# Kernel tuning notes

Hardware: AMD Instinct MI355X
Metric: run time of the kernel (lower is better)

## Reference

```python
import jax, jax.numpy as jnp
import numpy as np

DIM = 1024
SCALE = DIM ** (-0.5)
TEMPERATURE = 1.0


def setup_inputs() -> dict:
    key = jax.random.key(0)
    ks = jax.random.split(key, 7)
    B, N, D = 8, 4096, DIM
    s = 1.0 / np.sqrt(D)
    return {
        "x": jax.random.normal(ks[0], (B, N, D), dtype=jnp.float32),
        "Wq": jax.random.normal(ks[1], (D, D), dtype=jnp.float32) * s,
        "bq": jax.random.normal(ks[2], (D,), dtype=jnp.float32) * 0.01,
        "Wk": jax.random.normal(ks[3], (D, D), dtype=jnp.float32) * s,
        "bk": jax.random.normal(ks[4], (D,), dtype=jnp.float32) * 0.01,
        "Wv": jax.random.normal(ks[5], (D, D), dtype=jnp.float32) * s,
        "bv": jax.random.normal(ks[6], (D,), dtype=jnp.float32) * 0.01,
    }


def reference(x, Wq, bq, Wk, bk, Wv, bv):
    B, N, D = x.shape
    # adaptive_avg_pool1d from N -> N//2 with N even == mean over adjacent pairs
    q_input = x.reshape(B, N // 2, 2, D).mean(axis=2)  # [B, N/2, D]
    # torch Linear: y = x @ W.T + b
    q = jnp.einsum("bmd,ed->bme", q_input, Wq) + bq      # [B, N/2, D]
    k = jnp.einsum("bnd,ed->bne", x, Wk) + bk            # [B, N, D]
    v = jnp.einsum("bnd,ed->bne", x, Wv) + bv            # [B, N, D]
    attn = jnp.einsum("bmd,bnd->bmn", q, k) * SCALE      # [B, N/2, N]
    attn = jax.nn.softmax(attn * TEMPERATURE, axis=-1)
    k_out = jnp.einsum("bmn,bnd->bmd", attn, v)          # [B, N/2, D]
    return (q, k_out, k_out)
```

## Files before the change

kernel.cpp:

```cpp
#include <hip/hip_runtime.h>
#include <hip/hip_bf16.h>
#include <cstddef>

typedef __attribute__((ext_vector_type(8))) short s16x8;
typedef __attribute__((ext_vector_type(4))) short s16x4;
typedef __attribute__((ext_vector_type(4))) float f32x4;

#define MFMA_BF16(a, b, c) __builtin_amdgcn_mfma_f32_16x16x32_bf16((a), (b), (c), 0, 0, 0)

__device__ __forceinline__ short f2bf(float f) {
    union { float f; unsigned u; } cv; cv.f = f;
    unsigned u = cv.u;
    unsigned r = (u + 0x7FFFu + ((u >> 16) & 1u)) >> 16;
    return (short)r;
}
__device__ __forceinline__ float bf2f(unsigned short u) {
    union { unsigned u; float f; } cv; cv.u = ((unsigned)u) << 16; return cv.f;
}

__device__ __forceinline__ void gl16(const void* g, void* l) {
    __builtin_amdgcn_global_load_lds(
        (const __attribute__((address_space(1))) void*)g,
        (__attribute__((address_space(3))) void*)l, 16, 0, 0);
}

template <int MODE>
__global__ __launch_bounds__(256, 2) void gemm_bf(
    const void* __restrict__ Ap, const short* __restrict__ Bp,
    const float* __restrict__ bias, const float* __restrict__ lvec,
    void* __restrict__ Cp, void* __restrict__ Cp2)
{
    constexpr int NT  = (MODE == 4) ? 64 : 16;
    constexpr int LDA = (MODE == 4) ? 4096 : 1024;
    constexpr int LDB = (MODE == 4) ? 4096 : 1024;

    __shared__ short As[128 * 64];
    __shared__ short Bs[128 * 64];
    const int tid = threadIdx.x;

    int bx, by, z;
    if constexpr (MODE == 1 || MODE == 3 || MODE == 4 || MODE == 5) {
        const int n = blockIdx.x;
        constexpr int NBY = (MODE == 1) ? 8 : 16;
        z = n & 7; const int m = n >> 3; by = m % NBY; bx = m / NBY;
    } else { bx = blockIdx.x; by = blockIdx.y; z = blockIdx.z; }

    const int w = tid >> 6, l = tid & 63, l15 = l & 15, lhi = l >> 4;
    const int wy = w >> 1, wx = w & 1;
    const int X = (l15 & 7) << 3;
    const int lr8 = l >> 3, cb = l & 7, scb = cb ^ lr8;

    size_t arow0 = (size_t)by * 128, brow0 = (size_t)bx * 128;
    if constexpr (MODE == 3 || MODE == 4 || MODE == 5) arow0 += (size_t)z * 2048;
    if constexpr (MODE == 1 || MODE == 3 || MODE == 5) brow0 += (size_t)z * 4096;
    if constexpr (MODE == 4) brow0 += (size_t)z * 1024;

    const short* Ab = (const short*)Ap;
    const float* Af = (const float*)Ap;

    const short* gA = Ab + (arow0 + w * 32 + lr8) * (size_t)LDA + scb * 8;
    const short* gB = Bp + (brow0 + w * 32 + lr8) * (size_t)LDB + scb * 8;

    f32x4 acc[4][4];
    #pragma unroll
    for (int m = 0; m < 4; ++m)
        #pragma unroll
        for (int n = 0; n < 4; ++n) acc[m][n] = (f32x4){0.f, 0.f, 0.f, 0.f};

    const int r0b = tid >> 3, cb8 = (tid & 7) * 8;
    const int r0f = tid >> 4, kcs = tid & 15;

    for (int kt = 0; kt < NT; ++kt) {
        #pragma unroll
        for (int i = 0; i < 4; ++i)
            gl16(gB + (size_t)(i * 8) * LDB + kt * 64, &Bs[(w * 32 + i * 8) * 64]);
        if constexpr (MODE == 2) {
            #pragma unroll
            for (int p = 0; p < 4; ++p) {
                const int r = r0b + p * 32;
                const size_t g = (arow0 + r) * 2048 + kt * 64 + cb8;
                s16x8 u0 = *(const s16x8*)(Ab + g);
                s16x8 u1 = *(const s16x8*)(Ab + g + 1024);
                s16x8 o;
                #pragma unroll
                for (int j = 0; j < 8; ++j)
                    o[j] = f2bf(0.5f * (bf2f((unsigned short)u0[j]) + bf2f((unsigned short)u1[j])));
                *(s16x8*)&As[r * 64 + (cb8 ^ ((r & 7) * 8))] = o;
            }
        } else if constexpr (MODE == 3) {
            const int k0 = kt * 64 + kcs * 4;
            #pragma unroll
            for (int p = 0; p < 8; ++p) {
                const int r = r0f + p * 16;
                float4 u = *(const float4*)(Af + (arow0 + r) * 1024 + k0);
                s16x4 sa = { f2bf(u.x * 0.03125f), f2bf(u.y * 0.03125f),
                             f2bf(u.z * 0.03125f), f2bf(u.w * 0.03125f) };
                *(s16x4*)&As[r * 64 + ((kcs * 4) ^ ((r & 7) * 8))] = sa;
            }
        } else {
            #pragma unroll
            for (int i = 0; i < 4; ++i)
                gl16(gA + (size_t)(i * 8) * LDA + kt * 64, &As[(w * 32 + i * 8) * 64]);
        }
        __syncthreads();
        #pragma unroll
        for (int kk = 0; kk < 2; ++kk) {
            const int e = (kk * 32 + lhi * 8) ^ X;
            s16x8 af[4], bfr[4];
            #pragma unroll
            for (int m = 0; m < 4; ++m)
                af[m] = *(const s16x8*)&As[(wy * 64 + m * 16 + l15) * 64 + e];
            #pragma unroll
            for (int n = 0; n < 4; ++n)
                bfr[n] = *(const s16x8*)&Bs[(wx * 64 + n * 16 + l15) * 64 + e];
            #pragma unroll
            for (int m = 0; m < 4; ++m)
                #pragma unroll
                for (int n = 0; n < 4; ++n)
                    acc[m][n] = MFMA_BF16(af[m], bfr[n], acc[m][n]);
        }
        __syncthreads();
    }

    #pragma unroll
    for (int m = 0; m < 4; ++m) {
        #pragma unroll
        for (int j = 0; j < 4; ++j) {
            const int rl = wy * 64 + m * 16 + lhi * 4 + j;
            const int grow = by * 128 + rl;
            float radd = 0.f, rmul = 1.f;
            if constexpr (MODE == 1) radd = bias[grow];
            if constexpr (MODE == 4) rmul = 1.0f / lvec[(size_t)z * 2048 + grow];
            #pragma unroll
            for (int n = 0; n < 4; ++n) {
                const int cl = wx * 64 + n * 16 + l15;
                const int gcol = bx * 128 + cl;
                float v = acc[m][n][j];
                if constexpr (MODE == 0) {
                    ((short*)Cp)[(size_t)grow * 1024 + gcol] = f2bf(v + bias[gcol]);
                } else if constexpr (MODE == 1) {
                    ((short*)Cp)[(size_t)z * 4194304 + (size_t)grow * 4096 + gcol] = f2bf(v + radd);
                } else if constexpr (MODE == 2) {
                    const float qv = v + bias[gcol];
                    ((float*)Cp)[(size_t)grow * 1024 + gcol] = qv;
                    if (Cp2 != nullptr)
                        ((short*)Cp2)[(size_t)grow * 1024 + gcol] = f2bf(qv * 0.03125f);
                } else if constexpr (MODE == 3 || MODE == 5) {
                    ((short*)Cp)[(size_t)z * 8388608 + (size_t)grow * 4096 + gcol] = f2bf(v);
                } else {
                    const size_t o = ((size_t)z * 2048 + grow) * 1024 + gcol;
                    const float ov = v * rmul;
                    ((float*)Cp)[o] = ov;
                    ((float*)Cp2)[o] = ov;
                }
            }
        }
    }
}

template <int MODE>
__global__ __launch_bounds__(256, 2) void gemm_f32(
    const float* __restrict__ Ap, const float* __restrict__ Bp,
    const float* __restrict__ bias, void* __restrict__ Cp, void* __restrict__ Cp2)
{
    constexpr int LDA = (MODE == 2) ? 2048 : 1024;
    __shared__ short As[128 * 64];
    __shared__ short Bs[128 * 64];
    const int tid = threadIdx.x;
    const int bx = blockIdx.x, by = blockIdx.y, z = blockIdx.z;
    const int w = tid >> 6, l = tid & 63, l15 = l & 15, lhi = l >> 4;
    const int wy = w >> 1, wx = w & 1;
    const int X = (l15 & 7) << 3;

    size_t arow0 = (size_t)by * 128, brow0 = (size_t)bx * 128;
    if constexpr (MODE == 1) brow0 += (size_t)z * 4096;

    f32x4 acc[4][4];
    #pragma unroll
    for (int m = 0; m < 4; ++m)
        #pragma unroll
        for (int n = 0; n < 4; ++n) acc[m][n] = (f32x4){0.f, 0.f, 0.f, 0.f};

    const int r0f = tid >> 4, kcs = tid & 15;
    float4 ra[8], ra2[8], rb[8];

    auto load_tile = [&](int kt) {
        const int k0 = kt * 64 + kcs * 4;
        #pragma unroll
        for (int p = 0; p < 8; ++p) {
            const int r = r0f + p * 16;
            if constexpr (MODE == 2) {
                const float* s0 = Ap + (arow0 + r) * (size_t)LDA + k0;
                ra[p] = *(const float4*)s0;
                ra2[p] = *(const float4*)(s0 + 1024);
            } else {
                ra[p] = *(const float4*)(Ap + (arow0 + r) * (size_t)LDA + k0);
            }
            rb[p] = *(const float4*)(Bp + (brow0 + r) * (size_t)1024 + k0);
        }
    };

    load_tile(0);
    for (int kt = 0; kt < 16; ++kt) {
        #pragma unroll
        for (int p = 0; p < 8; ++p) {
            const int r = r0f + p * 16;
            const int e = (kcs * 4) ^ ((r & 7) << 3);
            float ax, ay, az, aw;
            if constexpr (MODE == 2) {
                ax = 0.5f * (ra[p].x + ra2[p].x); ay = 0.5f * (ra[p].y + ra2[p].y);
                az = 0.5f * (ra[p].z + ra2[p].z); aw = 0.5f * (ra[p].w + ra2[p].w);
            } else {
                ax = ra[p].x; ay = ra[p].y; az = ra[p].z; aw = ra[p].w;
            }
            s16x4 sa = { f2bf(ax), f2bf(ay), f2bf(az), f2bf(aw) };
            *(s16x4*)&As[r * 64 + e] = sa;
            s16x4 sb = { f2bf(rb[p].x), f2bf(rb[p].y), f2bf(rb[p].z), f2bf(rb[p].w) };
            *(s16x4*)&Bs[r * 64 + e] = sb;
        }
        if (kt + 1 < 16) load_tile(kt + 1);
        __syncthreads();
        #pragma unroll
        for (int kk = 0; kk < 2; ++kk) {
            const int e = (kk * 32 + lhi * 8) ^ X;
            s16x8 af[4], bfr[4];
            #pragma unroll
            for (int m = 0; m < 4; ++m)
                af[m] = *(const s16x8*)&As[(wy * 64 + m * 16 + l15) * 64 + e];
            #pragma unroll
            for (int n = 0; n < 4; ++n)
                bfr[n] = *(const s16x8*)&Bs[(wx * 64 + n * 16 + l15) * 64 + e];
            #pragma unroll
            for (int m = 0; m < 4; ++m)
                #pragma unroll
                for (int n = 0; n < 4; ++n)
                    acc[m][n] = MFMA_BF16(af[m], bfr[n], acc[m][n]);
        }
        __syncthreads();
    }

    #pragma unroll
    for (int m = 0; m < 4; ++m) {
        #pragma unroll
        for (int j = 0; j < 4; ++j) {
            const int rl = wy * 64 + m * 16 + lhi * 4 + j;
            const int grow = by * 128 + rl;
            const float radd = (MODE == 1) ? bias[grow] : 0.f;
            #pragma unroll
            for (int n = 0; n < 4; ++n) {
                const int cl = wx * 64 + n * 16 + l15;
                const int gcol = bx * 128 + cl;
                float v = acc[m][n][j];
                if constexpr (MODE == 0) {
                    ((short*)Cp)[(size_t)grow * 1024 + gcol] = f2bf(v + bias[gcol]);
                } else if constexpr (MODE == 1) {
                    ((short*)Cp)[(size_t)z * 4194304 + (size_t)grow * 4096 + gcol] = f2bf(v + radd);
                } else {
                    const float q = v + bias[gcol];
                    ((float*)Cp)[(size_t)grow * 1024 + gcol] = q;
                    ((short*)Cp2)[(size_t)grow * 1024 + gcol] = f2bf(q * 0.03125f);
                }
            }
        }
    }
}

__global__ __launch_bounds__(256, 4) void convert_x(const float* __restrict__ x,
                                                    short* __restrict__ xb)
{
    const size_t i0 = ((size_t)blockIdx.x * 256 + threadIdx.x) * 8;
    float4 a = *(const float4*)(x + i0), b = *(const float4*)(x + i0 + 4);
    s16x8 o = { f2bf(a.x), f2bf(a.y), f2bf(a.z), f2bf(a.w),
                f2bf(b.x), f2bf(b.y), f2bf(b.z), f2bf(b.w) };
    *(s16x8*)(xb + i0) = o;
}

__global__ __launch_bounds__(256, 4) void convert_w(
    const float* __restrict__ Wq, const float* __restrict__ Wk,
    const float* __restrict__ Wv, short* __restrict__ Wb)
{
    const int gid = blockIdx.x * 256 + threadIdx.x;
    const int seg = gid >> 17;
    const size_t off = (size_t)(gid & 131071) * 8;
    const float* s = (seg == 0) ? Wq : ((seg == 1) ? Wk : Wv);
    float4 a = *(const float4*)(s + off), b = *(const float4*)(s + off + 4);
    s16x8 o = { f2bf(a.x), f2bf(a.y), f2bf(a.z), f2bf(a.w),
                f2bf(b.x), f2bf(b.y), f2bf(b.z), f2bf(b.w) };
    *(s16x8*)(Wb + (size_t)seg * 1048576 + off) = o;
}

__global__ __launch_bounds__(256, 4) void softmax_rows(
    const unsigned short* __restrict__ Sin, unsigned short* __restrict__ Pout,
    float* __restrict__ lvec)
{
    const int w = threadIdx.x >> 6, l = threadIdx.x & 63;
    const int row = blockIdx.x * 4 + w;
    const unsigned short* rp = Sin + (size_t)row * 4096;
    unsigned short* wp = Pout + (size_t)row * 4096;

    s16x8 v[8];
    #pragma unroll
    for (int c = 0; c < 8; ++c)
        v[c] = *(const s16x8*)(rp + (c * 64 + l) * 8);

    float mx = -1e30f;
    #pragma unroll
    for (int c = 0; c < 8; ++c)
        #pragma unroll
        for (int j = 0; j < 8; ++j)
            mx = fmaxf(mx, bf2f((unsigned short)v[c][j]));
    #pragma unroll
    for (int d = 1; d < 64; d <<= 1) mx = fmaxf(mx, __shfl_xor(mx, d));

    float sum = 0.f;
    #pragma unroll
    for (int c = 0; c < 8; ++c) {
        #pragma unroll
        for (int j = 0; j < 8; ++j) {
            const float p = __expf(bf2f((unsigned short)v[c][j]) - mx);
            sum += p;
            v[c][j] = f2bf(p);
        }
    }
    #pragma unroll
    for (int d = 1; d < 64; d <<= 1) sum += __shfl_xor(sum, d);

    #pragma unroll
    for (int c = 0; c < 8; ++c)
        *(s16x8*)(wp + (c * 64 + l) * 8) = v[c];
    if (l == 0) lvec[row] = sum;
}

__global__ __launch_bounds__(256, 4) void dup_out(
    const float4* __restrict__ O, float4* __restrict__ o1, float4* __restrict__ o2)
{
    const size_t i0 = (size_t)blockIdx.x * 256 + threadIdx.x;
    #pragma unroll
    for (int p = 0; p < 4; ++p) {
        const size_t i = i0 + (size_t)p * 1048576;
        const float4 t = O[i];
        o1[i] = t;
        o2[i] = t;
    }
}

extern "C" void kernel_launch(void* const* d_in, const int* in_sizes, int n_in,
                              void* d_out, int out_size, void* d_ws, size_t ws_size,
                              hipStream_t stream) {
    const float* x  = (const float*)d_in[0];
    const float* Wq = (const float*)d_in[1];
    const float* bq = (const float*)d_in[2];
    const float* Wk = (const float*)d_in[3];
    const float* bk = (const float*)d_in[4];
    const float* Wv = (const float*)d_in[5];
    const float* bv = (const float*)d_in[6];

    float* out   = (float*)d_out;
    float* q_out = out;
    float* out1  = out + (size_t)16777216;
    float* out2  = out + (size_t)33554432;
    short* Smat  = (short*)out1;

    const unsigned long long NEED_A2 = 241434624ULL;
    const unsigned long long NEED_A1 = 207683584ULL;

    if ((unsigned long long)ws_size >= NEED_A2) {
        short* xb  = (short*)d_ws;
        short* Wb  = xb + (size_t)33554432;
        short* kws = Wb + (size_t)3145728;
        short* vT  = kws + (size_t)33554432;
        short* qs  = vT + (size_t)33554432;
        float* lws = (float*)(qs + (size_t)16777216);
        unsigned short* Pws = (unsigned short*)d_ws;

        convert_x<<<dim3(16384, 1, 1), 256, 0, stream>>>(x, xb);
        convert_w<<<dim3(1536, 1, 1), 256, 0, stream>>>(Wq, Wk, Wv, Wb);
        gemm_bf<0><<<dim3(8, 256, 1), 256, 0, stream>>>(xb, Wb + 1048576, bk, nullptr, (void*)kws, nullptr);
        gemm_bf<1><<<dim3(2048, 1, 1), 256, 0, stream>>>(Wb + 2097152, xb, bv, nullptr, (void*)vT, nullptr);
        gemm_bf<2><<<dim3(8, 128, 1), 256, 0, stream>>>(xb, Wb, bq, nullptr, (void*)q_out, (void*)qs);
        gemm_bf<5><<<dim3(4096, 1, 1), 256, 0, stream>>>(qs, kws, nullptr, nullptr, (void*)Smat, nullptr);
        softmax_rows<<<dim3(4096, 1, 1), 256, 0, stream>>>((const unsigned short*)Smat, Pws, lws);
        gemm_bf<4><<<dim3(1024, 1, 1), 256, 0, stream>>>(Pws, vT, nullptr, lws, (void*)out1, (void*)out2);
    } else if ((unsigned long long)ws_size >= NEED_A1) {
        short* xb  = (short*)d_ws;
        short* Wb  = xb + (size_t)33554432;
        short* kws = Wb + (size_t)3145728;
        short* vT  = kws + (size_t)33554432;
        float* lws = (float*)((char*)d_ws + 207618048ULL);
        unsigned short* Pws = (unsigned short*)d_ws;

        convert_x<<<dim3(16384, 1, 1), 256, 0, stream>>>(x, xb);
        convert_w<<<dim3(1536, 1, 1), 256, 0, stream>>>(Wq, Wk, Wv, Wb);
        gemm_bf<0><<<dim3(8, 256, 1), 256, 0, stream>>>(xb, Wb + 1048576, bk, nullptr, (void*)kws, nullptr);
        gemm_bf<1><<<dim3(2048, 1, 1), 256, 0, stream>>>(Wb + 2097152, xb, bv, nullptr, (void*)vT, nullptr);
        gemm_bf<2><<<dim3(8, 128, 1), 256, 0, stream>>>(xb, Wb, bq, nullptr, (void*)q_out, nullptr);
        gemm_bf<3><<<dim3(4096, 1, 1), 256, 0, stream>>>(q_out, kws, nullptr, nullptr, (void*)Smat, nullptr);
        softmax_rows<<<dim3(4096, 1, 1), 256, 0, stream>>>((const unsigned short*)Smat, Pws, lws);
        gemm_bf<4><<<dim3(1024, 1, 1), 256, 0, stream>>>(Pws, vT, nullptr, lws, (void*)out1, (void*)out2);
    } else {
        short* kws = (short*)d_ws;
        short* vT  = kws + (size_t)33554432;
        short* qs  = vT + (size_t)33554432;
        float* lws = (float*)((char*)d_ws + 167772160ULL);
        float* Ows = (float*)d_ws;

        gemm_f32<0><<<dim3(8, 256, 1), 256, 0, stream>>>(x, Wk, bk, (void*)kws, nullptr);
        gemm_f32<1><<<dim3(32, 8, 8), 256, 0, stream>>>(Wv, x, bv, (void*)vT, nullptr);
        gemm_f32<2><<<dim3(8, 128, 1), 256, 0, stream>>>(x, Wq, bq, (void*)q_out, (void*)qs);
        gemm_bf<5><<<dim3(4096, 1, 1), 256, 0, stream>>>(qs, kws, nullptr, nullptr, (void*)Smat, nullptr);
        softmax_rows<<<dim3(4096, 1, 1), 256, 0, stream>>>((const unsigned short*)Smat, (unsigned short*)Smat, lws);
        gemm_bf<4><<<dim3(1024, 1, 1), 256, 0, stream>>>(Smat, vT, nullptr, lws, (void*)Ows, (void*)Ows);
        dup_out<<<dim3(4096, 1, 1), 256, 0, stream>>>((const float4*)Ows, (float4*)out1, (float4*)out2);
    }
}
```

Baseline: 652.8 us.

## Add 256x256-tile double-buffered bf16 GEMM for attention score and PV products

Introduces a 512-thread GEMM kernel with 256x256 output tiles, a double-buffered LDS staging pipeline fed by direct global-to-LDS loads, and XOR-swizzled LDS addressing. It replaces the 128-tile kernels for the Q·K^T score product and the normalized P·V output product on the large-workspace path. The larger tiles raise operand reuse per loaded byte and cut global traffic. In exchange the kernel uses about 128KB of LDS and many accumulator registers, which limits occupancy. The P·V grid is only 256 blocks, so load balance across CUs may suffer.

```diff
diff --git a/kernel.cpp b/kernel.cpp
--- a/kernel.cpp
+++ b/kernel.cpp
@@ -22,6 +22,123 @@
     __builtin_amdgcn_global_load_lds(
         (const __attribute__((address_space(1))) void*)g,
         (__attribute__((address_space(3))) void*)l, 16, 0, 0);
+}
+
+template <int MODE>
+__global__ __launch_bounds__(512, 2) void gemm256(
+    const short* __restrict__ Ap, const short* __restrict__ Bp,
+    const float* __restrict__ lvec, void* __restrict__ Cp, void* __restrict__ Cp2)
+{
+    constexpr int NT  = (MODE == 1) ? 64 : 16;
+    constexpr int LDA = (MODE == 1) ? 4096 : 1024;
+    constexpr int LDB = (MODE == 1) ? 4096 : 1024;
+    constexpr int NBX = (MODE == 1) ? 4 : 16;
+
+    __shared__ short As[2][256 * 64];
+    __shared__ short Bs[2][256 * 64];
+
+    const int tid = threadIdx.x;
+    const int n = blockIdx.x;
+    const int z = n & 7;
+    const int m_ = n >> 3;
+    const int by = m_ & 7, bx = m_ >> 3;
+    (void)NBX;
+
+    const int w = tid >> 6, l = tid & 63;
+    const int l15 = l & 15, lhi = l >> 4;
+    const int wr = w >> 2, wc = w & 3;
+    const int X = (l15 & 7) << 3;
+    const int lr8 = l >> 3, cb = l & 7, scb = cb ^ lr8;
+
+    const size_t arow0 = (size_t)z * 2048 + (size_t)by * 256;
+    const size_t brow0 = (size_t)((MODE == 1) ? z * 1024 : z * 4096) + (size_t)bx * 256;
+
+    const short* gA = Ap + (arow0 + w * 8 + lr8) * (size_t)LDA + scb * 8;
+    const short* gB = Bp + (brow0 + w * 8 + lr8) * (size_t)LDB + scb * 8;
+
+    f32x4 acc[8][4];
+    #pragma unroll
+    for (int mm = 0; mm < 8; ++mm)
+        #pragma unroll
+        for (int nn = 0; nn < 4; ++nn) acc[mm][nn] = (f32x4){0.f, 0.f, 0.f, 0.f};
+
+    auto STAGE = [&](int c, int t) {
+        const size_t ko = (size_t)t * 64;
+        #pragma unroll
+        for (int i = 0; i < 4; ++i)
+            gl16(gA + (size_t)(i * 64) * LDA + ko, &As[c][(i * 64 + w * 8) * 64]);
+        #pragma unroll
+        for (int i = 0; i < 4; ++i)
+            gl16(gB + (size_t)(i * 64) * LDB + ko, &Bs[c][(i * 64 + w * 8) * 64]);
+    };
+
+    auto COMPUTE = [&](int c) {
+        #pragma unroll
+        for (int kk = 0; kk < 2; ++kk) {
+            const int e = (kk * 32 + lhi * 8) ^ X;
+            s16x8 af[8], bfr[4];
+            #pragma unroll
+            for (int mm = 0; mm < 8; ++mm)
+                af[mm] = *(const s16x8*)&As[c][(wr * 128 + mm * 16 + l15) * 64 + e];
+            #pragma unroll
+            for (int nn = 0; nn < 4; ++nn)
+                bfr[nn] = *(const s16x8*)&Bs[c][(wc * 64 + nn * 16 + l15) * 64 + e];
+            #pragma unroll
+            for (int mm = 0; mm < 8; ++mm)
+                #pragma unroll
+                for (int nn = 0; nn < 4; ++nn)
+                    acc[mm][nn] = MFMA_BF16(af[mm], bfr[nn], acc[mm][nn]);
+        }
+    };
+
+    STAGE(0, 0);
+    STAGE(1, 1);
+    asm volatile("s_waitcnt vmcnt(8)" ::: "memory");
+    __builtin_amdgcn_s_barrier();
+    asm volatile("" ::: "memory");
+
+    for (int t = 0; t < NT - 2; ++t) {
+        const int c = t & 1;
+        COMPUTE(c);
+        asm volatile("s_waitcnt lgkmcnt(0)" ::: "memory");
+        __builtin_amdgcn_s_barrier();
+        asm volatile("" ::: "memory");
+        __builtin_amdgcn_sched_barrier(0);
+        STAGE(c, t + 2);
+        asm volatile("s_waitcnt vmcnt(8)" ::: "memory");
+        __builtin_amdgcn_s_barrier();
+        asm volatile("" ::: "memory");
+    }
+    COMPUTE((NT - 2) & 1);
+    asm volatile("s_waitcnt vmcnt(0)" ::: "memory");
+    __builtin_amdgcn_s_barrier();
+    asm volatile("" ::: "memory");
+    COMPUTE((NT - 1) & 1);
+
+    #pragma unroll
+    for (int mm = 0; mm < 8; ++mm) {
+        #pragma unroll
+        for (int j = 0; j < 4; ++j) {
+            const int gr = by * 256 + wr * 128 + mm * 16 + lhi * 4 + j;
+            if constexpr (MODE == 0) {
+                #pragma unroll
+                for (int nn = 0; nn < 4; ++nn) {
+                    const int gc = bx * 256 + wc * 64 + nn * 16 + l15;
+                    ((short*)Cp)[(size_t)z * 8388608 + (size_t)gr * 4096 + gc] = f2bf(acc[mm][nn][j]);
+                }
+            } else {
+                const float rmul = 1.0f / lvec[(size_t)z * 2048 + gr];
+                #pragma unroll
+                for (int nn = 0; nn < 4; ++nn) {
+                    const int gc = bx * 256 + wc * 64 + nn * 16 + l15;
+                    const size_t o = ((size_t)z * 2048 + gr) * 1024 + gc;
+                    const float ov = acc[mm][nn][j] * rmul;
+                    ((float*)Cp)[o] = ov;
+                    ((float*)Cp2)[o] = ov;
+                }
+            }
+        }
+    }
 }
 
 template <int MODE>
@@ -378,9 +495,9 @@
         gemm_bf<0><<<dim3(8, 256, 1), 256, 0, stream>>>(xb, Wb + 1048576, bk, nullptr, (void*)kws, nullptr);
         gemm_bf<1><<<dim3(2048, 1, 1), 256, 0, stream>>>(Wb + 2097152, xb, bv, nullptr, (void*)vT, nullptr);
         gemm_bf<2><<<dim3(8, 128, 1), 256, 0, stream>>>(xb, Wb, bq, nullptr, (void*)q_out, (void*)qs);
-        gemm_bf<5><<<dim3(4096, 1, 1), 256, 0, stream>>>(qs, kws, nullptr, nullptr, (void*)Smat, nullptr);
+        gemm256<0><<<dim3(1024, 1, 1), 512, 0, stream>>>(qs, kws, nullptr, (void*)Smat, nullptr);
         softmax_rows<<<dim3(4096, 1, 1), 256, 0, stream>>>((const unsigned short*)Smat, Pws, lws);
-        gemm_bf<4><<<dim3(1024, 1, 1), 256, 0, stream>>>(Pws, vT, nullptr, lws, (void*)out1, (void*)out2);
+        gemm256<1><<<dim3(256, 1, 1), 512, 0, stream>>>((const short*)Pws, vT, lws, (void*)out1, (void*)out2);
     } else if ((unsigned long long)ws_size >= NEED_A1) {
         short* xb  = (short*)d_ws;
         short* Wb  = xb + (size_t)33554432;
```

Result: slower. 674.9 us (+3.4%).

## Add double-buffered LDS GEMM kernel and use it for K, V, S, PV GEMMs

Applied to the files above, without the earlier changes.

Introduces gemm_db, a variant of the bf16 MFMA GEMM that keeps two LDS buffers for A and B tiles. It issues async global-to-LDS loads for the next K tile before computing the current one, with one barrier per iteration. The goal is to overlap memory latency with MFMA work. The cost is double the LDS (64 KB per block), which may limit occupancy to two blocks per CU or fewer. The Q projection GEMM keeps the old kernel.

```diff
diff --git a/kernel.cpp b/kernel.cpp
--- a/kernel.cpp
+++ b/kernel.cpp
@@ -22,6 +22,114 @@
     __builtin_amdgcn_global_load_lds(
         (const __attribute__((address_space(1))) void*)g,
         (__attribute__((address_space(3))) void*)l, 16, 0, 0);
+}
+
+template <int MODE>
+__global__ __launch_bounds__(256, 2) void gemm_db(
+    const short* __restrict__ Ap, const short* __restrict__ Bp,
+    const float* __restrict__ bias, const float* __restrict__ lvec,
+    void* __restrict__ Cp, void* __restrict__ Cp2)
+{
+    constexpr int NT  = (MODE == 4) ? 64 : 16;
+    constexpr int LDA = (MODE == 4) ? 4096 : 1024;
+    constexpr int LDB = (MODE == 4) ? 4096 : 1024;
+
+    __shared__ short As[2][128 * 64];
+    __shared__ short Bs[2][128 * 64];
+
+    const int tid = threadIdx.x;
+    int bx, by, z;
+    if constexpr (MODE == 1 || MODE == 4 || MODE == 5) {
+        const int n = blockIdx.x;
+        constexpr int NBY = (MODE == 1) ? 8 : 16;
+        z = n & 7; const int m = n >> 3; by = m % NBY; bx = m / NBY;
+    } else { bx = blockIdx.x; by = blockIdx.y; z = 0; }
+
+    const int w = tid >> 6, l = tid & 63, l15 = l & 15, lhi = l >> 4;
+    const int wy = w >> 1, wx = w & 1;
+    const int X = (l15 & 7) << 3;
+    const int lr8 = l >> 3, cb = l & 7, scb = cb ^ lr8;
+
+    size_t arow0 = (size_t)by * 128, brow0 = (size_t)bx * 128;
+    if constexpr (MODE == 4 || MODE == 5) arow0 += (size_t)z * 2048;
+    if constexpr (MODE == 1 || MODE == 5) brow0 += (size_t)z * 4096;
+    if constexpr (MODE == 4) brow0 += (size_t)z * 1024;
+
+    const short* gA = Ap + (arow0 + w * 32 + lr8) * (size_t)LDA + scb * 8;
+    const short* gB = Bp + (brow0 + w * 32 + lr8) * (size_t)LDB + scb * 8;
+
+    f32x4 acc[4][4];
+    #pragma unroll
+    for (int m = 0; m < 4; ++m)
+        #pragma unroll
+        for (int n = 0; n < 4; ++n) acc[m][n] = (f32x4){0.f, 0.f, 0.f, 0.f};
+
+    auto STAGE = [&](int c, int t) {
+        const size_t ko = (size_t)t * 64;
+        #pragma unroll
+        for (int i = 0; i < 4; ++i)
+            gl16(gA + (size_t)(i * 8) * LDA + ko, &As[c][(w * 32 + i * 8) * 64]);
+        #pragma unroll
+        for (int i = 0; i < 4; ++i)
+            gl16(gB + (size_t)(i * 8) * LDB + ko, &Bs[c][(w * 32 + i * 8) * 64]);
+    };
+
+    auto COMPUTE = [&](int c) {
+        #pragma unroll
+        for (int kk = 0; kk < 2; ++kk) {
+            const int e = (kk * 32 + lhi * 8) ^ X;
+            s16x8 af[4], bfr[4];
+            #pragma unroll
+            for (int m = 0; m < 4; ++m)
+                af[m] = *(const s16x8*)&As[c][(wy * 64 + m * 16 + l15) * 64 + e];
+            #pragma unroll
+            for (int n = 0; n < 4; ++n)
+                bfr[n] = *(const s16x8*)&Bs[c][(wx * 64 + n * 16 + l15) * 64 + e];
+            #pragma unroll
+            for (int m = 0; m < 4; ++m)
+                #pragma unroll
+                for (int n = 0; n < 4; ++n)
+                    acc[m][n] = MFMA_BF16(af[m], bfr[n], acc[m][n]);
+        }
+    };
+
+    STAGE(0, 0);
+    __syncthreads();
+    for (int t = 0; t < NT; ++t) {
+        if (t + 1 < NT) STAGE((t + 1) & 1, t + 1);
+        COMPUTE(t & 1);
+        __syncthreads();
+    }
+
+    #pragma unroll
+    for (int m = 0; m < 4; ++m) {
+        #pragma unroll
+        for (int j = 0; j < 4; ++j) {
+            const int rl = wy * 64 + m * 16 + lhi * 4 + j;
+            const int grow = by * 128 + rl;
+            float radd = 0.f, rmul = 1.f;
+            if constexpr (MODE == 1) radd = bias[grow];
+            if constexpr (MODE == 4) rmul = 1.0f / lvec[(size_t)z * 2048 + grow];
+            #pragma unroll
+            for (int n = 0; n < 4; ++n) {
+                const int cl = wx * 64 + n * 16 + l15;
+                const int gcol = bx * 128 + cl;
+                float v = acc[m][n][j];
+                if constexpr (MODE == 0) {
+                    ((short*)Cp)[(size_t)grow * 1024 + gcol] = f2bf(v + bias[gcol]);
+                } else if constexpr (MODE == 1) {
+                    ((short*)Cp)[(size_t)z * 4194304 + (size_t)grow * 4096 + gcol] = f2bf(v + radd);
+                } else if constexpr (MODE == 5) {
+                    ((short*)Cp)[(size_t)z * 8388608 + (size_t)grow * 4096 + gcol] = f2bf(v);
+                } else {
+                    const size_t o = ((size_t)z * 2048 + grow) * 1024 + gcol;
+                    const float ov = v * rmul;
+                    ((float*)Cp)[o] = ov;
+                    ((float*)Cp2)[o] = ov;
+                }
+            }
+        }
+    }
 }
 
 template <int MODE>
@@ -375,12 +483,12 @@
 
         convert_x<<<dim3(16384, 1, 1), 256, 0, stream>>>(x, xb);
         convert_w<<<dim3(1536, 1, 1), 256, 0, stream>>>(Wq, Wk, Wv, Wb);
-        gemm_bf<0><<<dim3(8, 256, 1), 256, 0, stream>>>(xb, Wb + 1048576, bk, nullptr, (void*)kws, nullptr);
-        gemm_bf<1><<<dim3(2048, 1, 1), 256, 0, stream>>>(Wb + 2097152, xb, bv, nullptr, (void*)vT, nullptr);
+        gemm_db<0><<<dim3(8, 256, 1), 256, 0, stream>>>(xb, Wb + 1048576, bk, nullptr, (void*)kws, nullptr);
+        gemm_db<1><<<dim3(2048, 1, 1), 256, 0, stream>>>(Wb + 2097152, xb, bv, nullptr, (void*)vT, nullptr);
         gemm_bf<2><<<dim3(8, 128, 1), 256, 0, stream>>>(xb, Wb, bq, nullptr, (void*)q_out, (void*)qs);
-        gemm_bf<5><<<dim3(4096, 1, 1), 256, 0, stream>>>(qs, kws, nullptr, nullptr, (void*)Smat, nullptr);
+        gemm_db<5><<<dim3(4096, 1, 1), 256, 0, stream>>>(qs, kws, nullptr, nullptr, (void*)Smat, nullptr);
         softmax_rows<<<dim3(4096, 1, 1), 256, 0, stream>>>((const unsigned short*)Smat, Pws, lws);
-        gemm_bf<4><<<dim3(1024, 1, 1), 256, 0, stream>>>(Pws, vT, nullptr, lws, (void*)out1, (void*)out2);
+        gemm_db<4><<<dim3(1024, 1, 1), 256, 0, stream>>>((const short*)Pws, vT, nullptr, lws, (void*)out1, (void*)out2);
     } else if ((unsigned long long)ws_size >= NEED_A1) {
         short* xb  = (short*)d_ws;
         short* Wb  = xb + (size_t)33554432;
```

After: 774.3 us. 18.6% more time.

## Load A operand directly from global into registers for attention GEMMs

Applied to the files above, without the earlier changes.

Adds a gemm_ad kernel that reads the A tile (Q or P rows) straight from global memory into MFMA fragments and stages only the B tile through LDS with a swizzled layout. It is used for the QK^T score GEMM and the PV GEMM on the large-workspace path. This halves LDS usage and removes the A-side LDS writes and reads. In exchange, A fragment loads are uncoalesced, strided per-lane global reads with no double buffering, so memory latency may be exposed.

```diff
diff --git a/kernel.cpp b/kernel.cpp
--- a/kernel.cpp
+++ b/kernel.cpp
@@ -22,6 +22,94 @@
     __builtin_amdgcn_global_load_lds(
         (const __attribute__((address_space(1))) void*)g,
         (__attribute__((address_space(3))) void*)l, 16, 0, 0);
+}
+
+template <int MODE>
+__global__ __launch_bounds__(256, 2) void gemm_ad(
+    const short* __restrict__ Ap, const short* __restrict__ Bp,
+    const float* __restrict__ lvec, void* __restrict__ Cp, void* __restrict__ Cp2)
+{
+    constexpr int NT  = (MODE == 1) ? 64 : 16;
+    constexpr int LDA = (MODE == 1) ? 4096 : 1024;
+    constexpr int LDB = (MODE == 1) ? 4096 : 1024;
+
+    __shared__ short Bs[128 * 64];
+
+    const int tid = threadIdx.x;
+    const int n = blockIdx.x;
+    const int z = n & 7;
+    const int m_ = n >> 3;
+    const int by = m_ % 16, bx = m_ / 16;
+
+    const int w = tid >> 6, l = tid & 63, l15 = l & 15, lhi = l >> 4;
+    const int wy = w >> 1, wx = w & 1;
+    const int X = (l15 & 7) << 3;
+    const int lr8 = l >> 3, cb = l & 7, scb = cb ^ lr8;
+
+    const size_t arow0 = (size_t)z * 2048 + (size_t)by * 128;
+    const size_t brow0 = (size_t)bx * 128 + (size_t)((MODE == 1) ? z * 1024 : z * 4096);
+
+    const short* gB = Bp + (brow0 + w * 32 + lr8) * (size_t)LDB + scb * 8;
+    const short* aBase = Ap + (arow0 + wy * 64 + l15) * (size_t)LDA + lhi * 8;
+
+    f32x4 acc[4][4];
+    #pragma unroll
+    for (int m = 0; m < 4; ++m)
+        #pragma unroll
+        for (int nn = 0; nn < 4; ++nn) acc[m][nn] = (f32x4){0.f, 0.f, 0.f, 0.f};
+
+    for (int kt = 0; kt < NT; ++kt) {
+        s16x8 af[2][4];
+        #pragma unroll
+        for (int kk = 0; kk < 2; ++kk)
+            #pragma unroll
+            for (int m = 0; m < 4; ++m)
+                af[kk][m] = *(const s16x8*)(aBase + (size_t)(m * 16) * LDA + kt * 64 + kk * 32);
+        #pragma unroll
+        for (int i = 0; i < 4; ++i)
+            gl16(gB + (size_t)(i * 8) * LDB + kt * 64, &Bs[(w * 32 + i * 8) * 64]);
+        __syncthreads();
+        #pragma unroll
+        for (int kk = 0; kk < 2; ++kk) {
+            const int e = (kk * 32 + lhi * 8) ^ X;
+            s16x8 bfr[4];
+            #pragma unroll
+            for (int nn = 0; nn < 4; ++nn)
+                bfr[nn] = *(const s16x8*)&Bs[(wx * 64 + nn * 16 + l15) * 64 + e];
+            #pragma unroll
+            for (int m = 0; m < 4; ++m)
+                #pragma unroll
+                for (int nn = 0; nn < 4; ++nn)
+                    acc[m][nn] = MFMA_BF16(af[kk][m], bfr[nn], acc[m][nn]);
+        }
+        __syncthreads();
+    }
+
+    #pragma unroll
+    for (int m = 0; m < 4; ++m) {
+        #pragma unroll
+        for (int j = 0; j < 4; ++j) {
+            const int rl = wy * 64 + m * 16 + lhi * 4 + j;
+            const int grow = by * 128 + rl;
+            if constexpr (MODE == 0) {
+                #pragma unroll
+                for (int nn = 0; nn < 4; ++nn) {
+                    const int gcol = bx * 128 + wx * 64 + nn * 16 + l15;
+                    ((short*)Cp)[(size_t)z * 8388608 + (size_t)grow * 4096 + gcol] = f2bf(acc[m][nn][j]);
+                }
+            } else {
+                const float rmul = 1.0f / lvec[(size_t)z * 2048 + grow];
+                #pragma unroll
+                for (int nn = 0; nn < 4; ++nn) {
+                    const int gcol = bx * 128 + wx * 64 + nn * 16 + l15;
+                    const size_t o = ((size_t)z * 2048 + grow) * 1024 + gcol;
+                    const float ov = acc[m][nn][j] * rmul;
+                    ((float*)Cp)[o] = ov;
+                    ((float*)Cp2)[o] = ov;
+                }
+            }
+        }
+    }
 }
 
 template <int MODE>
@@ -378,9 +466,9 @@
         gemm_bf<0><<<dim3(8, 256, 1), 256, 0, stream>>>(xb, Wb + 1048576, bk, nullptr, (void*)kws, nullptr);
         gemm_bf<1><<<dim3(2048, 1, 1), 256, 0, stream>>>(Wb + 2097152, xb, bv, nullptr, (void*)vT, nullptr);
         gemm_bf<2><<<dim3(8, 128, 1), 256, 0, stream>>>(xb, Wb, bq, nullptr, (void*)q_out, (void*)qs);
-        gemm_bf<5><<<dim3(4096, 1, 1), 256, 0, stream>>>(qs, kws, nullptr, nullptr, (void*)Smat, nullptr);
+        gemm_ad<0><<<dim3(4096, 1, 1), 256, 0, stream>>>(qs, kws, nullptr, (void*)Smat, nullptr);
         softmax_rows<<<dim3(4096, 1, 1), 256, 0, stream>>>((const unsigned short*)Smat, Pws, lws);
-        gemm_bf<4><<<dim3(1024, 1, 1), 256, 0, stream>>>(Pws, vT, nullptr, lws, (void*)out1, (void*)out2);
+        gemm_ad<1><<<dim3(1024, 1, 1), 256, 0, stream>>>((const short*)Pws, vT, lws, (void*)out1, (void*)out2);
     } else if ((unsigned long long)ws_size >= NEED_A1) {
         short* xb  = (short*)d_ws;
         short* Wb  = xb + (size_t)33554432;
```

Measured after the change: 901.6 us. 38.1% more time.
